# Kernel tuning notes

Measured on AMD Instinct MI355X. Metric: run time of the kernel, lower is better.

The kernel has to match this reference:

```python
import jax, jax.numpy as jnp
import numpy as np

N, K, D, H = 16384, 8, 128, 256  # nodes, preds per node, emb dim, hidden


def _build_graph():
    i = np.arange(1, N + 1)[:, None]      # [N,1] node ids 1..N
    k = np.arange(K)[None, :]             # [1,K]
    pred = i - 1 - k                       # predecessor node ids
    mask = pred >= 0
    pred_nodes = np.maximum(pred, 0).astype(np.int32)        # [N,K]
    end = np.repeat(np.arange(1, N + 1), K).astype(np.int32)  # [N*K]
    edges = np.stack([pred_nodes.reshape(-1), end], axis=1)   # [E,2]
    pred_edge_idx = (np.arange(N * K).reshape(N, K) + 1).astype(np.int32)  # +1: zero row prepended to distances
    return pred_nodes, pred_edge_idx, mask, edges.astype(np.int32)


def setup_inputs() -> dict:
    key = jax.random.key(0)
    k1, k2, k3 = jax.random.split(key, 3)
    pred_nodes, pred_edge_idx, mask, edges = _build_graph()
    s1 = 1.0 / np.sqrt(2 * D)
    s2 = 1.0 / np.sqrt(H)
    return {
        "words_embs": jax.random.normal(k1, (N + 1, D), dtype=jnp.float32),
        "W1": jax.random.uniform(k2, (2 * D, H), jnp.float32, -s1, s1),
        "b1": jnp.zeros((H,), jnp.float32),
        "W2": jax.random.uniform(k3, (H, 1), jnp.float32, -s2, s2),
        "b2": jnp.zeros((1,), jnp.float32),
        "best_idxs": jnp.arange(N + 1, dtype=jnp.int32),  # the chain path 0->1->...->N
        "edges": jnp.asarray(edges),
        "pred_nodes": jnp.asarray(pred_nodes),
        "pred_edge_idx": jnp.asarray(pred_edge_idx),
        "pred_mask": jnp.asarray(mask),
    }


def _distance(x, y, W1, b1, W2, b2):
    # MLP over concatenated pair features: Linear -> Tanh -> Linear -> Softplus
    h = jnp.tanh(jnp.concatenate([x, y], axis=-1) @ W1 + b1)
    return jax.nn.softplus(h @ W2 + b2)  # [...,1]


def _forward_alg(words_embs, edges, pred_nodes, pred_edge_idx, pred_mask, W1, b1, W2, b2):
    n_nodes = pred_nodes.shape[0]
    d = _distance(words_embs[edges[:, 0]], words_embs[edges[:, 1]], W1, b1, W2, b2)  # [E,1]
    dists = jnp.concatenate([jnp.zeros((1, 1), d.dtype), d], axis=0)[:, 0]  # [E+1]
    esum0 = jnp.zeros((n_nodes + 1,), d.dtype)
    neg_inf = jnp.asarray(-jnp.inf, d.dtype)

    def step(esum, inp):
        i, preds, eidx, m = inp
        vals = jnp.where(m, esum[preds] - dists[eidx], neg_inf)  # [K]
        mx = jnp.max(vals)
        lse = mx + jnp.log(jnp.sum(jnp.exp(vals - mx)))
        return esum.at[i].set(lse), None

    idxs = jnp.arange(1, n_nodes + 1, dtype=jnp.int32)
    esum, _ = jax.lax.scan(step, esum0, (idxs, pred_nodes, pred_edge_idx, pred_mask))
    return esum[-1]


def reference(words_embs, W1, b1, W2, b2, best_idxs, edges, pred_nodes, pred_edge_idx, pred_mask):
    # gold path score
    feats = words_embs[best_idxs]  # [P,D]
    gold = _distance(feats[:-1], feats[1:], W1, b1, W2, b2).sum(0)  # [1]
    # partition-function-like forward score over the lattice
    fwd = _forward_alg(words_embs, edges, pred_nodes, pred_edge_idx, pred_mask, W1, b1, W2, b2)
    return (gold + fwd).mean()  # single-sample version of loss_fuc
```

## Files before the change

kernel.cpp:

```cpp
#include <hip/hip_runtime.h>
#include <math.h>

#define NNODES 16384
#define NV 16385
#define NEDGE 131072
#define NEG -1e30f
#define SCALE 2.8853900817779268f

typedef __attribute__((ext_vector_type(8))) short short8;
typedef __attribute__((ext_vector_type(8))) unsigned short ushort8;
typedef __attribute__((ext_vector_type(4))) float f32x4;

__device__ float g_part[4 * NEDGE];
__device__ float g_mats[32 * 64];
__device__ float g_gold;
__device__ int g_done;

__device__ __forceinline__ unsigned short f2bf(float x) {
  union { float f; unsigned int u; } c; c.f = x;
  unsigned int u = c.u;
  unsigned int r = (u + 0x7fffu + ((u >> 16) & 1u)) >> 16;
  return (unsigned short)r;
}
__device__ __forceinline__ float bf2f(unsigned short u) {
  union { unsigned int u; float f; } c; c.u = ((unsigned int)u) << 16;
  return c.f;
}

__device__ __forceinline__ float lse8(float x0, float x1, float x2, float x3,
                                      float x4, float x5, float x6, float x7) {
  float m = fmaxf(fmaxf(fmaxf(x0, x1), fmaxf(x2, x3)),
                  fmaxf(fmaxf(x4, x5), fmaxf(x6, x7)));
  float s = __expf(x0 - m) + __expf(x1 - m) + __expf(x2 - m) + __expf(x3 - m) +
            __expf(x4 - m) + __expf(x5 - m) + __expf(x6 - m) + __expf(x7 - m);
  return m + __logf(s);
}

__device__ __forceinline__ float comb8(float A, float B, int i8, int j) {
  float x0 = __shfl(A, i8 + 0) + __shfl(B, 0 + j);
  float x1 = __shfl(A, i8 + 1) + __shfl(B, 8 + j);
  float x2 = __shfl(A, i8 + 2) + __shfl(B, 16 + j);
  float x3 = __shfl(A, i8 + 3) + __shfl(B, 24 + j);
  float x4 = __shfl(A, i8 + 4) + __shfl(B, 32 + j);
  float x5 = __shfl(A, i8 + 5) + __shfl(B, 40 + j);
  float x6 = __shfl(A, i8 + 6) + __shfl(B, 48 + j);
  float x7 = __shfl(A, i8 + 7) + __shfl(B, 56 + j);
  return lse8(x0, x1, x2, x3, x4, x5, x6, x7);
}

__global__ __launch_bounds__(256, 5) void k12_fused(const float* __restrict__ emb,
                                                    const float* __restrict__ W1,
                                                    const float* __restrict__ b1,
                                                    const float* __restrict__ W2) {
  __shared__ __align__(16) unsigned short lds[15072];
  unsigned short* Es  = lds;
  unsigned short* WtA = lds + 5760;
  unsigned short* WtB = lds + 10368;
  unsigned short* CA  = lds;
  unsigned short* CB  = lds + 5760;
  unsigned short* W2s = lds + 14976;
  float* Wsum = (float*)(lds + 15040);

  const int t = threadIdx.x;
  const int h0 = blockIdx.x << 6;
  const int i0 = blockIdx.y << 6;
  const int wv = t >> 6, lane = t & 63;
  const int l15 = lane & 15, quad = lane >> 4;

  if (t < 64) W2s[t] = f2bf(-2.f * W2[h0 + t]);
  if (t < 8) {
    float s = 0.f;
#pragma unroll
    for (int jj = 0; jj < 8; ++jj) s += W2[h0 + (t << 3) + jj];
    Wsum[t] = s;
  }

  f32x4 accA[5], accB[4];
#pragma unroll
  for (int m = 0; m < 5; ++m) accA[m] = (f32x4){0.f, 0.f, 0.f, 0.f};
#pragma unroll
  for (int m = 0; m < 4; ++m) accB[m] = (f32x4){0.f, 0.f, 0.f, 0.f};

  for (int hk = 0; hk < 2; ++hk) {
    if (hk) __syncthreads();
#pragma unroll
    for (int it = 0; it < 5; ++it) {
      int idx = t + (it << 8);
      int row = idx >> 4;
      int k4 = (idx & 15) << 2;
      int v = i0 - 7 + row;
      float4 g = make_float4(0.f, 0.f, 0.f, 0.f);
      if (v >= 0 && v < NV) g = *(const float4*)&emb[v * 128 + (hk << 6) + k4];
      uint2 pk;
      pk.x = f2bf(g.x) | ((unsigned int)f2bf(g.y) << 16);
      pk.y = f2bf(g.z) | ((unsigned int)f2bf(g.w) << 16);
      *(uint2*)&Es[row * 72 + k4] = pk;
    }
    {
      const int n = t & 63;
      const int kg = (t >> 6) << 4;
#pragma unroll
      for (int kk = 0; kk < 16; kk += 2) {
        int k = (hk << 6) + kg + kk;
        float a0 = W1[k * 256 + h0 + n];
        float a1 = W1[(k + 1) * 256 + h0 + n];
        *(unsigned int*)&WtA[n * 72 + kg + kk] = f2bf(a0) | ((unsigned int)f2bf(a1) << 16);
        float c0 = W1[(128 + k) * 256 + h0 + n];
        float c1 = W1[(128 + k + 1) * 256 + h0 + n];
        *(unsigned int*)&WtB[n * 72 + kg + kk] = f2bf(c0) | ((unsigned int)f2bf(c1) << 16);
      }
    }
    __syncthreads();
    const int kq = quad << 3;
#pragma unroll
    for (int kc = 0; kc < 2; ++kc) {
      const int kb = (kc << 5) + kq;
      short8 fA = *(const short8*)&WtA[((wv << 4) + l15) * 72 + kb];
      short8 fB = *(const short8*)&WtB[((wv << 4) + l15) * 72 + kb];
#pragma unroll
      for (int mf = 0; mf < 5; ++mf) {
        short8 a = *(const short8*)&Es[((mf << 4) + l15) * 72 + kb];
        accA[mf] = __builtin_amdgcn_mfma_f32_16x16x32_bf16(a, fA, accA[mf], 0, 0, 0);
      }
#pragma unroll
      for (int mf = 0; mf < 4; ++mf) {
        short8 a = *(const short8*)&Es[(8 + (mf << 4) + l15) * 72 + kb];
        accB[mf] = __builtin_amdgcn_mfma_f32_16x16x32_bf16(a, fB, accB[mf], 0, 0, 0);
      }
    }
  }
  __syncthreads();
  const int hcol = (wv << 4) + l15;
  const float b1s = b1[h0 + hcol];
#pragma unroll
  for (int mf = 0; mf < 5; ++mf) {
    int rb = (mf << 4) + (quad << 2);
#pragma unroll
    for (int rr = 0; rr < 4; ++rr)
      CA[(rb + rr) * 72 + hcol] = f2bf((accA[mf][rr] + b1s) * SCALE);
  }
#pragma unroll
  for (int mf = 0; mf < 4; ++mf) {
    int rb = (mf << 4) + (quad << 2);
#pragma unroll
    for (int rr = 0; rr < 4; ++rr)
      CB[(rb + rr) * 72 + hcol] = f2bf(accB[mf][rr] * SCALE);
  }
  __syncthreads();
  const int k = t & 7;
  const int qb = t >> 3;
  float part[2] = {0.f, 0.f};
#pragma unroll
  for (int g = 0; g < 8; ++g) {
    const int s = (g + (k << 1)) & 7;
    ushort8 wv8 = *(const ushort8*)&W2s[s << 3];
    float m2w[8];
#pragma unroll
    for (int jj = 0; jj < 8; ++jj) m2w[jj] = bf2f(wv8[jj]);
    const float ws = Wsum[s];
#pragma unroll
    for (int j = 0; j < 2; ++j) {
      const int q = qb + (j << 5);
      ushort8 a8 = *(const ushort8*)&CA[(7 + q - k) * 72 + (s << 3)];
      ushort8 b8 = *(const ushort8*)&CB[q * 72 + (s << 3)];
      float p = part[j];
#pragma unroll
      for (int jj = 0; jj < 8; ++jj) {
        float x = bf2f(a8[jj]) + bf2f(b8[jj]);
        float e = __builtin_amdgcn_exp2f(x);
        float r = __builtin_amdgcn_rcpf(e + 1.f);
        p = fmaf(r, m2w[jj], p);
      }
      part[j] = p + ws;
    }
  }
  const int ebase = blockIdx.x * NEDGE + (blockIdx.y << 9) + t;
  g_part[ebase] = part[0];
  g_part[ebase + 256] = part[1];
}

__global__ __launch_bounds__(256) void k_tail(const float* __restrict__ b2,
                                              float* __restrict__ out) {
  __shared__ float wf[64][64];
  __shared__ float red[256];
  __shared__ float m8[8][64];
  __shared__ float l2m[4][64];
  __shared__ int s_tick;
  const int t = threadIdx.x;
  const int b = blockIdx.x;
  const float b2v = b2[0];
  float gold = 0.f;
#pragma unroll
  for (int it = 0; it < 4; ++it) {
    const int e4 = t + (it << 8);
    const int gidx = (b << 10) + e4;
    float4 s0 = *(const float4*)&g_part[gidx << 2];
    float4 s1 = *(const float4*)&g_part[NEDGE + (gidx << 2)];
    float4 s2 = *(const float4*)&g_part[2 * NEDGE + (gidx << 2)];
    float4 s3 = *(const float4*)&g_part[3 * NEDGE + (gidx << 2)];
    float d0 = s0.x + s1.x + s2.x + s3.x + b2v;
    float d1 = s0.y + s1.y + s2.y + s3.y + b2v;
    float d2 = s0.z + s1.z + s2.z + s3.z + b2v;
    float d3 = s0.w + s1.w + s2.w + s3.w + b2v;
    d0 = fmaxf(d0, 0.f) + log1pf(__expf(-fabsf(d0)));
    d1 = fmaxf(d1, 0.f) + log1pf(__expf(-fabsf(d1)));
    d2 = fmaxf(d2, 0.f) + log1pf(__expf(-fabsf(d2)));
    d3 = fmaxf(d3, 0.f) + log1pf(__expf(-fabsf(d3)));
    const int q = e4 << 2;
    const int cl = q >> 9, r = q & 511;
    const int s = r >> 3, kk = r & 7;
    *(float4*)&wf[s][(cl << 3) + kk] = make_float4(d0, d1, d2, d3);
    if ((t & 1) == 0) gold += d0;
  }
  red[t] = gold;
  __syncthreads();
  if (b == 0 && t == 0) {
    for (int s = 0; s < 7; ++s)
      for (int kk = s + 1; kk < 8; ++kk) wf[s][kk] = 1e30f;
  }
  for (int o = 128; o > 0; o >>= 1) {
    __syncthreads();
    if (t < o) red[t] += red[t + o];
  }
  __syncthreads();
  if (t == 0) atomicAdd(&g_gold, red[0]);
  if (t < 64) {
    const int g = t >> 3, j = t & 7;
    float P[8];
#pragma unroll
    for (int kk = 0; kk < 8; ++kk) P[kk] = (kk == j) ? 0.f : NEG;
    for (int s = 0; s < 64; ++s) {
      const float* wp = &wf[s][g << 3];
      float4 wa = *(const float4*)wp;
      float4 wb = *(const float4*)(wp + 4);
      float nv = lse8(P[0] - wa.x, P[1] - wa.y, P[2] - wa.z, P[3] - wa.w,
                      P[4] - wb.x, P[5] - wb.y, P[6] - wb.z, P[7] - wb.w);
#pragma unroll
      for (int kk = 7; kk > 0; --kk) P[kk] = P[kk - 1];
      P[0] = nv;
    }
#pragma unroll
    for (int kk = 0; kk < 8; ++kk) m8[g][(kk << 3) + j] = P[kk];
    const int i8 = (t >> 3) << 3;
    float R = m8[0][t];
#pragma unroll
    for (int g2 = 1; g2 < 8; ++g2) R = comb8(m8[g2][t], R, i8, j);
    g_mats[(b << 6) + t] = R;
  }
  __threadfence();
  __syncthreads();
  if (t == 0) s_tick = atomicAdd(&g_done, 1);
  __syncthreads();
  if (s_tick != 31) return;
  __threadfence();

  {
    const int l = t & 63, w = t >> 6;
    const int i8 = (l >> 3) << 3, j = l & 7;
    float G = g_mats[((w << 3) << 6) + l];
#pragma unroll
    for (int s2 = 1; s2 < 8; ++s2)
      G = comb8(g_mats[(((w << 3) + s2) << 6) + l], G, i8, j);
    l2m[w][l] = G;
    __syncthreads();
    if (t < 64) {
      float G2 = l2m[0][t];
#pragma unroll
      for (int w2 = 1; w2 < 4; ++w2) G2 = comb8(l2m[w2][t], G2, i8, j);
      if (t == 0) {
        out[0] = g_gold + G2;
        g_gold = 0.f;
        g_done = 0;
      }
    }
  }
}

extern "C" void kernel_launch(void* const* d_in, const int* in_sizes, int n_in,
                              void* d_out, int out_size, void* d_ws, size_t ws_size,
                              hipStream_t stream) {
  const float* emb = (const float*)d_in[0];
  const float* W1 = (const float*)d_in[1];
  const float* b1 = (const float*)d_in[2];
  const float* W2 = (const float*)d_in[3];
  const float* b2 = (const float*)d_in[4];
  float* out = (float*)d_out;
  hipLaunchKernelGGL(k12_fused, dim3(4, 256), dim3(256), 0, stream, emb, W1, b1, W2);
  hipLaunchKernelGGL(k_tail, dim3(32), dim3(256), 0, stream, b2, out);
}
```

Before: 117.7 us.

## Load W1 fragments directly into registers and stage full-K embeddings once

The W1 B-operand fragments are now read from global memory straight into registers instead of being staged through LDS. The embedding tile is loaded once for the full K=128 rather than in two halves. This removes the hk loop and one barrier and shrinks LDS so more blocks can be resident (launch bounds raised to 7). The cost is more live registers for the fragments and uncoalesced strided global reads of W1 per lane.

```diff
diff --git a/kernel.cpp b/kernel.cpp
--- a/kernel.cpp
+++ b/kernel.cpp
@@ -48,24 +48,23 @@
   return lse8(x0, x1, x2, x3, x4, x5, x6, x7);
 }
 
-__global__ __launch_bounds__(256, 5) void k12_fused(const float* __restrict__ emb,
+__global__ __launch_bounds__(256, 7) void k12_fused(const float* __restrict__ emb,
                                                     const float* __restrict__ W1,
                                                     const float* __restrict__ b1,
                                                     const float* __restrict__ W2) {
-  __shared__ __align__(16) unsigned short lds[15072];
+  __shared__ __align__(16) unsigned short lds[10960];
   unsigned short* Es  = lds;
-  unsigned short* WtA = lds + 5760;
-  unsigned short* WtB = lds + 10368;
   unsigned short* CA  = lds;
   unsigned short* CB  = lds + 5760;
-  unsigned short* W2s = lds + 14976;
-  float* Wsum = (float*)(lds + 15040);
+  unsigned short* W2s = lds + 10880;
+  float* Wsum = (float*)(lds + 10944);
 
   const int t = threadIdx.x;
   const int h0 = blockIdx.x << 6;
   const int i0 = blockIdx.y << 6;
   const int wv = t >> 6, lane = t & 63;
   const int l15 = lane & 15, quad = lane >> 4;
+  const int colh = h0 + (wv << 4) + l15;
 
   if (t < 64) W2s[t] = f2bf(-2.f * W2[h0 + t]);
   if (t < 8) {
@@ -75,58 +74,54 @@
     Wsum[t] = s;
   }
 
+#pragma unroll
+  for (int it = 0; it < 10; ++it) {
+    int idx = t + (it << 8);
+    int row = idx >> 5;
+    int k4 = (idx & 31) << 2;
+    int v = i0 - 7 + row;
+    float4 g = make_float4(0.f, 0.f, 0.f, 0.f);
+    if (v >= 0 && v < NV) g = *(const float4*)&emb[v * 128 + k4];
+    uint2 pk;
+    pk.x = f2bf(g.x) | ((unsigned int)f2bf(g.y) << 16);
+    pk.y = f2bf(g.z) | ((unsigned int)f2bf(g.w) << 16);
+    *(uint2*)&Es[row * 136 + k4] = pk;
+  }
+
   f32x4 accA[5], accB[4];
 #pragma unroll
   for (int m = 0; m < 5; ++m) accA[m] = (f32x4){0.f, 0.f, 0.f, 0.f};
 #pragma unroll
   for (int m = 0; m < 4; ++m) accB[m] = (f32x4){0.f, 0.f, 0.f, 0.f};
 
-  for (int hk = 0; hk < 2; ++hk) {
-    if (hk) __syncthreads();
-#pragma unroll
-    for (int it = 0; it < 5; ++it) {
-      int idx = t + (it << 8);
-      int row = idx >> 4;
-      int k4 = (idx & 15) << 2;
-      int v = i0 - 7 + row;
-      float4 g = make_float4(0.f, 0.f, 0.f, 0.f);
-      if (v >= 0 && v < NV) g = *(const float4*)&emb[v * 128 + (hk << 6) + k4];
-      uint2 pk;
-      pk.x = f2bf(g.x) | ((unsigned int)f2bf(g.y) << 16);
-      pk.y = f2bf(g.z) | ((unsigned int)f2bf(g.w) << 16);
-      *(uint2*)&Es[row * 72 + k4] = pk;
-    }
-    {
-      const int n = t & 63;
-      const int kg = (t >> 6) << 4;
-#pragma unroll
-      for (int kk = 0; kk < 16; kk += 2) {
-        int k = (hk << 6) + kg + kk;
-        float a0 = W1[k * 256 + h0 + n];
-        float a1 = W1[(k + 1) * 256 + h0 + n];
-        *(unsigned int*)&WtA[n * 72 + kg + kk] = f2bf(a0) | ((unsigned int)f2bf(a1) << 16);
-        float c0 = W1[(128 + k) * 256 + h0 + n];
-        float c1 = W1[(128 + k + 1) * 256 + h0 + n];
-        *(unsigned int*)&WtB[n * 72 + kg + kk] = f2bf(c0) | ((unsigned int)f2bf(c1) << 16);
-      }
-    }
-    __syncthreads();
-    const int kq = quad << 3;
-#pragma unroll
-    for (int kc = 0; kc < 2; ++kc) {
-      const int kb = (kc << 5) + kq;
-      short8 fA = *(const short8*)&WtA[((wv << 4) + l15) * 72 + kb];
-      short8 fB = *(const short8*)&WtB[((wv << 4) + l15) * 72 + kb];
-#pragma unroll
-      for (int mf = 0; mf < 5; ++mf) {
-        short8 a = *(const short8*)&Es[((mf << 4) + l15) * 72 + kb];
-        accA[mf] = __builtin_amdgcn_mfma_f32_16x16x32_bf16(a, fA, accA[mf], 0, 0, 0);
-      }
-#pragma unroll
-      for (int mf = 0; mf < 4; ++mf) {
-        short8 a = *(const short8*)&Es[(8 + (mf << 4) + l15) * 72 + kb];
-        accB[mf] = __builtin_amdgcn_mfma_f32_16x16x32_bf16(a, fB, accB[mf], 0, 0, 0);
-      }
+  short8 fA[4], fB[4];
+#pragma unroll
+  for (int kc = 0; kc < 4; ++kc) {
+    const int kb = (kc << 5) + (quad << 3);
+#pragma unroll
+    for (int i = 0; i < 8; i += 2) {
+      float a0 = W1[(kb + i) * 256 + colh];
+      float a1 = W1[(kb + i + 1) * 256 + colh];
+      float c0 = W1[(128 + kb + i) * 256 + colh];
+      float c1 = W1[(128 + kb + i + 1) * 256 + colh];
+      ((unsigned int*)&fA[kc])[i >> 1] = f2bf(a0) | ((unsigned int)f2bf(a1) << 16);
+      ((unsigned int*)&fB[kc])[i >> 1] = f2bf(c0) | ((unsigned int)f2bf(c1) << 16);
+    }
+  }
+  __syncthreads();
+
+#pragma unroll
+  for (int kc = 0; kc < 4; ++kc) {
+    const int kbase = (kc << 5) + (quad << 3);
+#pragma unroll
+    for (int mf = 0; mf < 5; ++mf) {
+      short8 a = *(const short8*)&Es[((mf << 4) + l15) * 136 + kbase];
+      accA[mf] = __builtin_amdgcn_mfma_f32_16x16x32_bf16(a, fA[kc], accA[mf], 0, 0, 0);
+    }
+#pragma unroll
+    for (int mf = 0; mf < 4; ++mf) {
+      short8 a = *(const short8*)&Es[(8 + (mf << 4) + l15) * 136 + kbase];
+      accB[mf] = __builtin_amdgcn_mfma_f32_16x16x32_bf16(a, fB[kc], accB[mf], 0, 0, 0);
     }
   }
   __syncthreads();
```

New measurement: 118.6 us. About the same (+0.8%).
